# Kernel optimization log

Measured on AMD Instinct MI355X. Metric: run time of the kernel, lower is better.

Reference implementation:

```python
import jax, jax.numpy as jnp
import numpy as np

EPS = 1e-5

def masked_group_norm(x, mask, gamma, beta, num_groups):
    # x: [B,D,H,W,C] (zero at unoccupied), mask: [B,D,H,W,1] float
    B, D, H, W, C = x.shape
    G = num_groups
    Cg = C // G
    xg = x.reshape(B, -1, G, Cg)          # [B,V,G,Cg]
    m = mask.reshape(B, -1, 1, 1)         # [B,V,1,1]
    cnt = jnp.maximum(m.sum(axis=1, keepdims=True) * Cg, 1.0)  # elems per (B,G)
    mean = (xg * m).sum(axis=(1, 3), keepdims=True) / cnt
    var = (((xg - mean) ** 2) * m).sum(axis=(1, 3), keepdims=True) / cnt
    y = (xg - mean) * jax.lax.rsqrt(var + EPS)
    y = y.reshape(B, D, H, W, C)
    return (y * gamma + beta) * mask

def downsample2(x, mask):
    # mean-pool occupied children under coords//2; new site occupied if any child is
    B, D, H, W, C = x.shape
    xr = x.reshape(B, D // 2, 2, H // 2, 2, W // 2, 2, C)
    mr = mask.reshape(B, D // 2, 2, H // 2, 2, W // 2, 2, 1)
    cnt = mr.sum(axis=(2, 4, 6))
    y = xr.sum(axis=(2, 4, 6)) / jnp.maximum(cnt, 1.0)
    new_mask = (cnt > 0).astype(x.dtype)
    return y, new_mask

def subm_conv3d(x, w, b, mask):
    # submanifold conv: unoccupied inputs are zero; outputs only at occupied sites
    y = jax.lax.conv_general_dilated(
        x, w, window_strides=(1, 1, 1), padding='SAME',
        dimension_numbers=('NDHWC', 'DHWIO', 'NDHWC'))
    return (y + b) * mask

def setup_inputs() -> dict:
    key = jax.random.key(0)
    ks = jax.random.split(key, 12)
    B, D, C, Co = 4, 64, 64, 128
    x = jax.random.normal(ks[0], (B, D, D, D, C), dtype=jnp.float32)
    mask = jax.random.randint(ks[1], (B, D, D, D), 0, 2).astype(jnp.int32)
    s = 0.05
    return {
        'x': x, 'mask': mask,
        'gn1_w': jnp.ones((C,), jnp.float32), 'gn1_b': jnp.zeros((C,), jnp.float32),
        'w1': jax.random.normal(ks[2], (3, 3, 3, C, Co), jnp.float32) * s,
        'b1': jax.random.normal(ks[3], (Co,), jnp.float32) * s,
        'gn2_w': jnp.ones((Co,), jnp.float32), 'gn2_b': jnp.zeros((Co,), jnp.float32),
        'w2': jax.random.normal(ks[4], (3, 3, 3, Co, Co), jnp.float32) * s,
        'b2': jax.random.normal(ks[5], (Co,), jnp.float32) * s,
        'wskip': jax.random.normal(ks[6], (C, Co), jnp.float32) * s,
        'bskip': jax.random.normal(ks[7], (Co,), jnp.float32) * s,
    }

def reference(x, mask, gn1_w, gn1_b, w1, b1, gn2_w, gn2_b, w2, b2, wskip, bskip):
    NUM_GROUPS = 32
    m = mask.astype(x.dtype)[..., None]          # [B,D,H,W,1]
    x = x * m                                    # sparse tensor: zero off-mask
    # act_layers: SparseGroupNorm32 + SparseSiLU
    h = masked_group_norm(x, m, gn1_w, gn1_b, NUM_GROUPS)
    h = jax.nn.silu(h)                           # silu(0)=0, stays sparse
    # downsample both h and residual x
    h, dm = downsample2(h, m)
    xd, _ = downsample2(x, m)
    # out_layers: conv3 -> GN -> SiLU -> conv3
    h = subm_conv3d(h, w1, b1, dm)
    h = masked_group_norm(h, dm, gn2_w, gn2_b, NUM_GROUPS)
    h = jax.nn.silu(h)
    h = subm_conv3d(h, w2, b2, dm)
    # skip: 1x1 sparse conv (out_channels != channels)
    skip = (jnp.einsum('bdhwc,co->bdhwo', xd, wskip) + bskip) * dm
    return h + skip
```

## Files before the change

### kernel.cpp

```cpp
#include <hip/hip_runtime.h>
#include <cstdint>
#include <cstddef>

#define B_ 4
#define V1 262144
#define C1 64
#define V2 32768
#define C2 128
#define TOTV 131072
#define P_ 34
#define P2_ 1156
#define P3_ 39304
#define SBSTRIDE ((size_t)4 * P3_)

#define OFF_S1A 0
#define OFF_S2A 128
#define OFF_CNT1 256
#define OFF_S1B 260
#define OFF_S2B 388
#define OFF_CNT2 516

typedef __bf16 bf16x8 __attribute__((ext_vector_type(8)));
typedef float f32x4 __attribute__((ext_vector_type(4)));

__device__ __forceinline__ float bf2f(unsigned short u) {
    return __builtin_bit_cast(float, (unsigned)u << 16);
}
__device__ __forceinline__ unsigned short f2bf(float f) {
    unsigned u = __builtin_bit_cast(unsigned, f);
    u += 0x7fffu + ((u >> 16) & 1u);
    return (unsigned short)(u >> 16);
}

__device__ __forceinline__ void barrier_nodrain() {
    asm volatile("s_waitcnt lgkmcnt(0)" ::: "memory");
    __builtin_amdgcn_s_barrier();
}

__device__ __forceinline__ int a_ofs(int ks, int csh) {
    int s = ks & ((1 << csh) - 1), tap = ks >> csh;
    int dz = tap / 9, r = tap % 9, dy = r / 3, dx = r % 3;
    return s * (int)(SBSTRIDE * 64) + (dz * P2_ + dy * P_ + dx) * 64;
}

__global__ __launch_bounds__(256) void k0_wprep(const float* __restrict__ w1,
                                                const float* __restrict__ w2,
                                                const float* __restrict__ wskip,
                                                unsigned short* __restrict__ w1t,
                                                unsigned short* __restrict__ w2t,
                                                int* __restrict__ d1,
                                                int* __restrict__ d2)
{
    int i = blockIdx.x * 256 + threadIdx.x;
    if (blockIdx.x == 0) {
        int t = threadIdx.x;
        if (t < 54)               d1[t] = (t + 1 < 54)  ? a_ofs(t + 1, 1) - a_ofs(t, 1) : 0;
        if (t >= 64 && t < 172) { int j = t - 64;
                                  d2[j] = (j + 1 < 108) ? a_ofs(j + 1, 2) - a_ofs(j, 2) : 0; }
    }
    if (i < 54 * 4096) {
        int slab = i >> 12, r = i & 4095;
        int q = r >> 10, n = (r >> 3) & 127, j = r & 7;
        int t = slab >> 1, s = slab & 1;
        int ci = s * 32 + q * 8 + j;
        w1t[i] = f2bf(w1[((size_t)t * 64 + ci) * 128 + n]);
    }
    int i2 = i - 54 * 4096;
    if (i2 >= 0 && i2 < 110 * 4096) {
        int slab = i2 >> 12, r = i2 & 4095;
        int q = r >> 10, n = (r >> 3) & 127, j = r & 7;
        float v;
        if (slab < 108) {
            int t = slab >> 2, s = slab & 3;
            int ci = s * 32 + q * 8 + j;
            v = w2[((size_t)t * 128 + ci) * 128 + n];
        } else {
            int ci = (slab - 108) * 32 + q * 8 + j;
            v = wskip[(size_t)ci * 128 + n];
        }
        w2t[i2] = f2bf(v);
    }
}

__global__ __launch_bounds__(256) void kz_border(unsigned short* __restrict__ h1p,
                                                 unsigned short* __restrict__ h2p)
{
    int i = blockIdx.x * 256 + threadIdx.x;
    if (i >= 24 * P3_) return;
    int sb = i / P3_, vox = i % P3_;
    int vz = vox / P2_, r = vox % P2_, vy = r / P_, vx = r % P_;
    bool border = (vz == 0) | (vz == 33) | (vy == 0) | (vy == 33) | (vx == 0) | (vx == 33);
    if (!border) return;
    unsigned short* base = (sb < 8) ? (h1p + (size_t)sb * P3_ * 32 + (size_t)vox * 32)
                                    : (h2p + (size_t)(sb - 8) * P3_ * 32 + (size_t)vox * 32);
    uint4 z = {0, 0, 0, 0};
    uint4* b4 = (uint4*)base;
    b4[0] = z; b4[1] = z; b4[2] = z; b4[3] = z;
}

__global__ __launch_bounds__(256) void k1_stats1(const float* __restrict__ x,
                                                 const int* __restrict__ mask,
                                                 float* __restrict__ stats)
{
    __shared__ float ls1[32], ls2[32];
    __shared__ float lcnt;
    int tid = threadIdx.x;
    if (tid < 32) { ls1[tid] = 0.f; ls2[tid] = 0.f; }
    if (tid == 0) lcnt = 0.f;
    __syncthreads();

    int b  = blockIdx.x & 3;
    int bb = blockIdx.x >> 2;
    int c4 = tid & 15;
    int vl = tid >> 4;

    const float* xb = x + ((size_t)b * V1) * C1;
    const int*   mb = mask + (size_t)b * V1;

    float s1a = 0.f, s2a = 0.f, s1b = 0.f, s2b = 0.f, mc = 0.f;
    for (int ch = bb; ch < V1 / 16; ch += 1024) {
        int v = ch * 16 + vl;
        int m = mb[v];
        if (c4 == 0) mc += (float)m;
        if (m) {
            float4 xv = *(const float4*)(xb + (size_t)v * C1 + c4 * 4);
            s1a += xv.x + xv.y;  s2a += xv.x * xv.x + xv.y * xv.y;
            s1b += xv.z + xv.w;  s2b += xv.z * xv.z + xv.w * xv.w;
        }
    }
    atomicAdd(&ls1[2 * c4],     s1a); atomicAdd(&ls2[2 * c4],     s2a);
    atomicAdd(&ls1[2 * c4 + 1], s1b); atomicAdd(&ls2[2 * c4 + 1], s2b);
    if (c4 == 0) atomicAdd(&lcnt, mc);
    __syncthreads();
    if (tid < 32) {
        atomicAdd(&stats[OFF_S1A + b * 32 + tid], ls1[tid]);
        atomicAdd(&stats[OFF_S2A + b * 32 + tid], ls2[tid]);
    }
    if (tid == 0) atomicAdd(&stats[OFF_CNT1 + b], lcnt);
}

__global__ __launch_bounds__(256) void k2_down(const float* __restrict__ x,
                                               const int* __restrict__ mask,
                                               const float* __restrict__ gn1w,
                                               const float* __restrict__ gn1b,
                                               const float* __restrict__ stats,
                                               unsigned short* __restrict__ h1p,
                                               unsigned short* __restrict__ xdb,
                                               float* __restrict__ dm)
{
    int tid = threadIdx.x;
    int c  = tid & 63;
    int vl = tid >> 6;
    size_t ov = (size_t)blockIdx.x * 4 + vl;
    int b  = (int)(ov >> 15);
    int v2 = (int)(ov & 32767);
    int z = v2 >> 10, y = (v2 >> 5) & 31, xk = v2 & 31;

    int g = c >> 1;
    float ce   = fmaxf(stats[OFF_CNT1 + b] * 2.f, 1.f);
    float mean = stats[OFF_S1A + b * 32 + g] / ce;
    float var  = stats[OFF_S2A + b * 32 + g] / ce - mean * mean;
    float rinv = rsqrtf(var + 1e-5f);
    float a  = rinv * gn1w[c];
    float bc = gn1b[c] - mean * a;

    const int*   mb = mask + ((size_t)b << 18);
    const float* xb = x + (((size_t)b << 18) << 6);

    float hacc = 0.f, xacc = 0.f; int cnt = 0;
    #pragma unroll
    for (int dz = 0; dz < 2; ++dz)
    #pragma unroll
    for (int dy = 0; dy < 2; ++dy)
    #pragma unroll
    for (int dx = 0; dx < 2; ++dx) {
        int v1 = ((2 * z + dz) << 12) | ((2 * y + dy) << 6) | (2 * xk + dx);
        if (mb[v1]) {
            cnt++;
            float xv = xb[(size_t)v1 * 64 + c];
            xacc += xv;
            float yv = fmaf(xv, a, bc);
            hacc += yv / (1.f + expf(-yv));
        }
    }
    float inv = 1.f / fmaxf((float)cnt, 1.f);
    int pvox = (z + 1) * P2_ + (y + 1) * P_ + (xk + 1);
    size_t so = ((size_t)(c >> 5) * SBSTRIDE + (size_t)b * P3_ + pvox) * 32 + (c & 31);
    h1p[so] = f2bf(hacc * inv);
    xdb[ov * 64 + c] = f2bf(xacc * inv);
    if (c == 0) dm[ov] = (cnt > 0) ? 1.f : 0.f;
}

template<int CIN, bool SKIP>
__global__ __launch_bounds__(256, 4) void conv3_mfma(
    const unsigned short* __restrict__ srcP,
    const unsigned short* __restrict__ sksrc,
    const unsigned short* __restrict__ wT,
    const int* __restrict__ tblA,
    const float* __restrict__ bias,
    const float* __restrict__ bias2,
    const float* __restrict__ dm,
    float* __restrict__ outf,
    unsigned short* __restrict__ outb)
{
    constexpr int CS  = CIN / 32;
    constexpr int NKM = 27 * CS;
    constexpr int NK  = NKM + (SKIP ? 2 : 0);

    __shared__ short smem[2][4096];

    const int tid  = threadIdx.x;
    const int lane = tid & 63;
    const int wv   = tid >> 6;
    const int orig = blockIdx.x;
    const int blk  = (orig & 7) * 128 + (orig >> 3);
    const int b    = blk >> 8;
    const int z    = (blk >> 3) & 31;
    const int yo   = blk & 7;
    const int y0   = yo * 4 + wv;
    const int vb   = b * 32768;
    const int klo  = (lane >> 4) * 8;
    const int xl   = lane & 15;
    const int rlo  = (lane >> 4) * 4;

    const uint4* wT4 = (const uint4*)wT;
    uint4* sm4 = (uint4*)&smem[0][0];

    f32x4 acc[2][8];
    #pragma unroll
    for (int f = 0; f < 2; ++f)
        #pragma unroll
        for (int nb = 0; nb < 8; ++nb)
            acc[f][nb] = (f32x4){0.f, 0.f, 0.f, 0.f};

    const char* pA = (const char*)srcP +
        (((size_t)b * P3_ + (size_t)(z * P2_ + y0 * P_ + xl)) * 32 + klo) * 2;

    auto loadSkip = [&](int ss, bf16x8 af[2]) {
        const unsigned short* abase = sksrc + ss * 32;
        #pragma unroll
        for (int f = 0; f < 2; ++f) {
            int xx = f * 16 + xl;
            af[f] = *(const bf16x8*)(abase +
                     (size_t)(vb + z * 1024 + y0 * 32 + xx) * 64 + klo);
        }
    };

    {
        uint4 p0 = wT4[tid], p1 = wT4[tid + 256];
        sm4[tid] = p0; sm4[tid + 256] = p1;
    }
    bf16x8 afc[2];
    afc[0] = *(const bf16x8*)pA;
    afc[1] = *(const bf16x8*)(pA + 1024);
    pA += tblA[0];
    const uint4* wRun = wT4 + 1024 + tid;
    uint4 qn0 = {}, qn1 = {};
    if (NK > 1) { qn0 = wT4[512 + tid]; qn1 = wT4[512 + 256 + tid]; }
    barrier_nodrain();

    int cur = 0;
    #pragma unroll 2
    for (int ks = 0; ks < NK; ++ks) {
        bf16x8 afn[2] = {{}, {}};
        if (ks + 1 < NKM) {
            afn[0] = *(const bf16x8*)pA;
            afn[1] = *(const bf16x8*)(pA + 1024);
            pA += tblA[ks + 1];
        } else if (SKIP && ks + 1 < NK) {
            loadSkip(ks + 1 - NKM, afn);
        }
        uint4 r0 = {}, r1 = {};
        if (ks + 2 < NK) { r0 = wRun[0]; r1 = wRun[256]; }
        wRun += 512;
        const int eoffb = cur * 4096 + ((lane >> 4) * 128 + xl) * 8;
        #pragma unroll
        for (int nb = 0; nb < 8; ++nb) {
            bf16x8 bfr = *(const bf16x8*)(&smem[0][0] + eoffb + nb * 128);
            acc[0][nb] = __builtin_amdgcn_mfma_f32_16x16x32_bf16(afc[0], bfr, acc[0][nb], 0, 0, 0);
            acc[1][nb] = __builtin_amdgcn_mfma_f32_16x16x32_bf16(afc[1], bfr, acc[1][nb], 0, 0, 0);
        }
        if (ks + 1 < NK) {
            sm4[(cur ^ 1) * 512 + tid] = qn0;
            sm4[(cur ^ 1) * 512 + 256 + tid] = qn1;
        }
        barrier_nodrain();
        afc[0] = afn[0]; afc[1] = afn[1];
        qn0 = r0; qn1 = r1;
        cur ^= 1;
    }

    float bv[8];
    #pragma unroll
    for (int nb = 0; nb < 8; ++nb) {
        int co = nb * 16 + xl;
        if constexpr (SKIP) bv[nb] = bias[co] + bias2[co];
        else                bv[nb] = bias[co];
    }
    #pragma unroll
    for (int f = 0; f < 2; ++f) {
        int xb2 = f * 16 + rlo;
        #pragma unroll
        for (int j = 0; j < 4; ++j) {
            int vox = vb + z * 1024 + y0 * 32 + xb2 + j;
            float dmx = dm[vox];
            #pragma unroll
            for (int nb = 0; nb < 8; ++nb) {
                float o = (acc[f][nb][j] + bv[nb]) * dmx;
                if constexpr (SKIP) outf[(size_t)vox * 128 + nb * 16 + xl] = o;
                else                outb[(size_t)vox * 128 + nb * 16 + xl] = f2bf(o);
            }
        }
    }
}

__global__ __launch_bounds__(256) void k4_stats2(const unsigned short* __restrict__ h2a,
                                                 const float* __restrict__ dm,
                                                 float* __restrict__ stats)
{
    __shared__ float ls1[32], ls2[32];
    __shared__ float lcnt;
    int tid = threadIdx.x;
    if (tid < 32) { ls1[tid] = 0.f; ls2[tid] = 0.f; }
    if (tid == 0) lcnt = 0.f;
    __syncthreads();

    int b  = blockIdx.x & 3;
    int bb = blockIdx.x >> 2;
    int g  = tid & 31;
    int vl = tid >> 5;

    const unsigned short* hb = h2a + ((size_t)b * V2) * C2;
    const float* dmb = dm + (size_t)b * V2;

    float s1 = 0.f, s2 = 0.f, mc = 0.f;
    for (int ch = bb; ch < V2 / 8; ch += 1024) {
        int v = ch * 8 + vl;
        float m = dmb[v];
        if (g == 0) mc += m;
        if (m != 0.f) {
            ushort4 hv = *(const ushort4*)(hb + (size_t)v * C2 + g * 4);
            float h0 = bf2f(hv.x), h1 = bf2f(hv.y), h2 = bf2f(hv.z), h3 = bf2f(hv.w);
            s1 += h0 + h1 + h2 + h3;
            s2 += h0 * h0 + h1 * h1 + h2 * h2 + h3 * h3;
        }
    }
    atomicAdd(&ls1[g], s1); atomicAdd(&ls2[g], s2);
    if (g == 0) atomicAdd(&lcnt, mc);
    __syncthreads();
    if (tid < 32) {
        atomicAdd(&stats[OFF_S1B + b * 32 + tid], ls1[tid]);
        atomicAdd(&stats[OFF_S2B + b * 32 + tid], ls2[tid]);
    }
    if (tid == 0) atomicAdd(&stats[OFF_CNT2 + b], lcnt);
}

__global__ __launch_bounds__(256) void k5_gn2(const unsigned short* __restrict__ h2a,
                                              unsigned short* __restrict__ h2p,
                                              const float* __restrict__ stats,
                                              const float* __restrict__ dm,
                                              const float* __restrict__ gn2w,
                                              const float* __restrict__ gn2b)
{
    int idx = blockIdx.x * 256 + threadIdx.x;
    int v = idx >> 5, g = idx & 31;
    int b = v >> 15;
    int v2 = v & 32767;
    float ce   = fmaxf(stats[OFF_CNT2 + b] * 4.f, 1.f);
    float mean = stats[OFF_S1B + b * 32 + g] / ce;
    float var  = stats[OFF_S2B + b * 32 + g] / ce - mean * mean;
    float rinv = rsqrtf(var + 1e-5f);
    float dmv  = dm[v];
    ushort4 hv = *(const ushort4*)(h2a + (size_t)idx * 4);
    float4 gw = *(const float4*)(gn2w + g * 4);
    float4 gb = *(const float4*)(gn2b + g * 4);
    float a, t;
    ushort4 o;
    a = rinv * gw.x; t = (fmaf(bf2f(hv.x), a, gb.x - mean * a)) * dmv; o.x = f2bf(t / (1.f + expf(-t)));
    a = rinv * gw.y; t = (fmaf(bf2f(hv.y), a, gb.y - mean * a)) * dmv; o.y = f2bf(t / (1.f + expf(-t)));
    a = rinv * gw.z; t = (fmaf(bf2f(hv.z), a, gb.z - mean * a)) * dmv; o.z = f2bf(t / (1.f + expf(-t)));
    a = rinv * gw.w; t = (fmaf(bf2f(hv.w), a, gb.w - mean * a)) * dmv; o.w = f2bf(t / (1.f + expf(-t)));
    int zz = v2 >> 10, yy = (v2 >> 5) & 31, xx = v2 & 31;
    int pvox = (zz + 1) * P2_ + (yy + 1) * P_ + (xx + 1);
    size_t so = ((size_t)(g >> 3) * SBSTRIDE + (size_t)b * P3_ + pvox) * 32 + (g & 7) * 4;
    *(ushort4*)(h2p + so) = o;
}

extern "C" void kernel_launch(void* const* d_in, const int* in_sizes, int n_in,
                              void* d_out, int out_size, void* d_ws, size_t ws_size,
                              hipStream_t stream)
{
    const float* x     = (const float*)d_in[0];
    const int*   mask  = (const int*)d_in[1];
    const float* gn1w  = (const float*)d_in[2];
    const float* gn1b  = (const float*)d_in[3];
    const float* w1    = (const float*)d_in[4];
    const float* b1    = (const float*)d_in[5];
    const float* gn2w  = (const float*)d_in[6];
    const float* gn2b  = (const float*)d_in[7];
    const float* w2    = (const float*)d_in[8];
    const float* b2    = (const float*)d_in[9];
    const float* wskip = (const float*)d_in[10];
    const float* bskip = (const float*)d_in[11];
    float* out = (float*)d_out;

    char* wsb = (char*)d_ws;
    float*          stats = (float*)wsb;
    float*          dm    = (float*)(wsb + 4096);
    unsigned short* h1p   = (unsigned short*)(wsb + 528384);
    unsigned short* xdb   = (unsigned short*)(wsb + 20652032);
    unsigned short* h2a   = (unsigned short*)(wsb + 37429248);
    unsigned short* h2p   = (unsigned short*)(wsb + 70983680);
    unsigned short* w1t   = (unsigned short*)(wsb + 111230976);
    unsigned short* w2t   = (unsigned short*)(wsb + 111673344);
    int*            d1    = (int*)(wsb + 112574464);
    int*            d2    = (int*)(wsb + 112574720);

    hipMemsetAsync(stats, 0, 520 * sizeof(float), stream);

    hipLaunchKernelGGL(k0_wprep, dim3(2624), dim3(256), 0, stream, w1, w2, wskip, w1t, w2t, d1, d2);
    hipLaunchKernelGGL(kz_border, dim3((24 * P3_ + 255) / 256), dim3(256), 0, stream, h1p, h2p);
    hipLaunchKernelGGL(k1_stats1, dim3(4096), dim3(256), 0, stream, x, mask, stats);
    hipLaunchKernelGGL(k2_down, dim3(32768), dim3(256), 0, stream,
                       x, mask, gn1w, gn1b, stats, h1p, xdb, dm);
    hipLaunchKernelGGL((conv3_mfma<64, false>), dim3(1024), dim3(256), 0, stream,
                       h1p, (const unsigned short*)nullptr, w1t, d1, b1, (const float*)nullptr,
                       dm, (float*)nullptr, h2a);
    hipLaunchKernelGGL(k4_stats2, dim3(4096), dim3(256), 0, stream, h2a, dm, stats);
    hipLaunchKernelGGL(k5_gn2, dim3(16384), dim3(256), 0, stream, h2a, h2p, stats, dm, gn2w, gn2b);
    hipLaunchKernelGGL((conv3_mfma<128, true>), dim3(1024), dim3(256), 0, stream,
                       h2p, xdb, w2t, d2, b2, bskip, dm, out, (unsigned short*)nullptr);
}
```

Before: 450.6 us.

## Stage conv weights via direct global-to-LDS loads, two K-steps per barrier

The MFMA conv main loop now processes two K-slices per phase, halving the number of barriers, and double-buffers a 16KB weight tile per phase. Weights are staged with global_load_lds (direct global-to-LDS DMA) instead of round-tripping through registers and ds_write. s_setprio brackets the MFMA block to favor the math waves. LDS use grows to 32KB per block, which may limit occupancy at 4 blocks per CU. The vmcnt(4) wait relies on the four A-fragment loads being issued after the LDS loads.

```diff
diff --git a/kernel.cpp b/kernel.cpp
--- a/kernel.cpp
+++ b/kernel.cpp
@@ -30,11 +30,6 @@
     unsigned u = __builtin_bit_cast(unsigned, f);
     u += 0x7fffu + ((u >> 16) & 1u);
     return (unsigned short)(u >> 16);
-}
-
-__device__ __forceinline__ void barrier_nodrain() {
-    asm volatile("s_waitcnt lgkmcnt(0)" ::: "memory");
-    __builtin_amdgcn_s_barrier();
 }
 
 __device__ __forceinline__ int a_ofs(int ks, int csh) {
@@ -203,11 +198,12 @@
     float* __restrict__ outf,
     unsigned short* __restrict__ outb)
 {
-    constexpr int CS  = CIN / 32;
-    constexpr int NKM = 27 * CS;
-    constexpr int NK  = NKM + (SKIP ? 2 : 0);
-
-    __shared__ short smem[2][4096];
+    constexpr int CS   = CIN / 32;
+    constexpr int NKM  = 27 * CS;
+    constexpr int NPHM = NKM / 2;
+    constexpr int NPH  = NPHM + (SKIP ? 1 : 0);
+
+    __shared__ short smem[2][8192];
 
     const int tid  = threadIdx.x;
     const int lane = tid & 63;
@@ -223,9 +219,6 @@
     const int xl   = lane & 15;
     const int rlo  = (lane >> 4) * 4;
 
-    const uint4* wT4 = (const uint4*)wT;
-    uint4* sm4 = (uint4*)&smem[0][0];
-
     f32x4 acc[2][8];
     #pragma unroll
     for (int f = 0; f < 2; ++f)
@@ -236,7 +229,7 @@
     const char* pA = (const char*)srcP +
         (((size_t)b * P3_ + (size_t)(z * P2_ + y0 * P_ + xl)) * 32 + klo) * 2;
 
-    auto loadSkip = [&](int ss, bf16x8 af[2]) {
+    auto loadSkip = [&](int ss, bf16x8* af) {
         const unsigned short* abase = sksrc + ss * 32;
         #pragma unroll
         for (int f = 0; f < 2; ++f) {
@@ -246,47 +239,59 @@
         }
     };
 
-    {
-        uint4 p0 = wT4[tid], p1 = wT4[tid + 256];
-        sm4[tid] = p0; sm4[tid + 256] = p1;
-    }
-    bf16x8 afc[2];
-    afc[0] = *(const bf16x8*)pA;
-    afc[1] = *(const bf16x8*)(pA + 1024);
-    pA += tblA[0];
-    const uint4* wRun = wT4 + 1024 + tid;
-    uint4 qn0 = {}, qn1 = {};
-    if (NK > 1) { qn0 = wT4[512 + tid]; qn1 = wT4[512 + 256 + tid]; }
-    barrier_nodrain();
+    auto stageW = [&](int pr, int buf) {
+        const char* g = (const char*)wT + (size_t)pr * 16384 + wv * 1024 + (lane << 4);
+        char* l = (char*)&smem[0][0] + buf * 16384 + wv * 1024;
+        #pragma unroll
+        for (int j = 0; j < 4; ++j)
+            __builtin_amdgcn_global_load_lds(
+                (const __attribute__((address_space(1))) unsigned int*)(g + j * 4096),
+                (__attribute__((address_space(3))) unsigned int*)(l + j * 4096),
+                16, 0, 0);
+    };
+
+    bf16x8 afc[4];
+    stageW(0, 0);
+    afc[0] = *(const bf16x8*)pA; afc[1] = *(const bf16x8*)(pA + 1024); pA += tblA[0];
+    afc[2] = *(const bf16x8*)pA; afc[3] = *(const bf16x8*)(pA + 1024); pA += tblA[1];
+    asm volatile("s_waitcnt vmcnt(4)" ::: "memory");
+    __builtin_amdgcn_s_barrier();
 
     int cur = 0;
     #pragma unroll 2
-    for (int ks = 0; ks < NK; ++ks) {
-        bf16x8 afn[2] = {{}, {}};
-        if (ks + 1 < NKM) {
-            afn[0] = *(const bf16x8*)pA;
-            afn[1] = *(const bf16x8*)(pA + 1024);
-            pA += tblA[ks + 1];
-        } else if (SKIP && ks + 1 < NK) {
-            loadSkip(ks + 1 - NKM, afn);
-        }
-        uint4 r0 = {}, r1 = {};
-        if (ks + 2 < NK) { r0 = wRun[0]; r1 = wRun[256]; }
-        wRun += 512;
-        const int eoffb = cur * 4096 + ((lane >> 4) * 128 + xl) * 8;
+    for (int p = 0; p < NPH; ++p) {
+        const bool more = (p + 1 < NPH);
+        bf16x8 afn[4] = {{}, {}, {}, {}};
+        if (more) {
+            stageW(p + 1, cur ^ 1);
+            if (2 * p + 2 < NKM) {
+                afn[0] = *(const bf16x8*)pA; afn[1] = *(const bf16x8*)(pA + 1024);
+                pA += tblA[2 * p + 2];
+                afn[2] = *(const bf16x8*)pA; afn[3] = *(const bf16x8*)(pA + 1024);
+                pA += tblA[2 * p + 3];
+            } else if (SKIP) {
+                loadSkip(0, &afn[0]);
+                loadSkip(1, &afn[2]);
+            }
+        }
+        __builtin_amdgcn_s_setprio(1);
         #pragma unroll
-        for (int nb = 0; nb < 8; ++nb) {
-            bf16x8 bfr = *(const bf16x8*)(&smem[0][0] + eoffb + nb * 128);
-            acc[0][nb] = __builtin_amdgcn_mfma_f32_16x16x32_bf16(afc[0], bfr, acc[0][nb], 0, 0, 0);
-            acc[1][nb] = __builtin_amdgcn_mfma_f32_16x16x32_bf16(afc[1], bfr, acc[1][nb], 0, 0, 0);
-        }
-        if (ks + 1 < NK) {
-            sm4[(cur ^ 1) * 512 + tid] = qn0;
-            sm4[(cur ^ 1) * 512 + 256 + tid] = qn1;
-        }
-        barrier_nodrain();
-        afc[0] = afn[0]; afc[1] = afn[1];
-        qn0 = r0; qn1 = r1;
+        for (int ss = 0; ss < 2; ++ss) {
+            const short* bp = &smem[0][0] + cur * 8192 + ss * 4096 +
+                              ((lane >> 4) * 128 + xl) * 8;
+            #pragma unroll
+            for (int nb = 0; nb < 8; ++nb) {
+                bf16x8 bfr = *(const bf16x8*)(bp + nb * 128);
+                acc[0][nb] = __builtin_amdgcn_mfma_f32_16x16x32_bf16(afc[ss * 2 + 0], bfr, acc[0][nb], 0, 0, 0);
+                acc[1][nb] = __builtin_amdgcn_mfma_f32_16x16x32_bf16(afc[ss * 2 + 1], bfr, acc[1][nb], 0, 0, 0);
+            }
+        }
+        __builtin_amdgcn_s_setprio(0);
+        if (more) asm volatile("s_waitcnt vmcnt(4)" ::: "memory");
+        else      asm volatile("s_waitcnt vmcnt(0)" ::: "memory");
+        asm volatile("s_waitcnt lgkmcnt(0)" ::: "memory");
+        __builtin_amdgcn_s_barrier();
+        afc[0] = afn[0]; afc[1] = afn[1]; afc[2] = afn[2]; afc[3] = afn[3];
         cur ^= 1;
     }
 
```

Measured after the change: 442.1 us. No clear change (-1.9%).
